# Performance work log

Hardware: AMD Instinct MI355X
Metric: run time of the kernel (lower is better)

The kernel has to match this reference:

```python
import jax, jax.numpy as jnp
import numpy as np

NEG_SLOPE = 0.2

def _gatv2_layer(x, src, tgt, Wl, Wr, att, bias, num_nodes, heads, ch):
    # x: [N, Fin]; src/tgt: [E] (self loops already included)
    xl = (x @ Wl).reshape(num_nodes, heads, ch)  # source transform [N,H,C]
    xr = (x @ Wr).reshape(num_nodes, heads, ch)  # target transform [N,H,C]
    m = xl[src] + xr[tgt]                        # [E,H,C]
    m = jnp.where(m > 0, m, NEG_SLOPE * m)       # LeakyReLU
    e = jnp.einsum('ehc,hc->eh', m, att)         # attention logits [E,H]
    # softmax over incoming edges of each target node (numerically stable)
    e_max = jax.ops.segment_max(e, tgt, num_segments=num_nodes)
    e_max = jnp.where(jnp.isfinite(e_max), e_max, 0.0)
    alpha = jnp.exp(e - e_max[tgt])              # [E,H]
    denom = jax.ops.segment_sum(alpha, tgt, num_segments=num_nodes)
    alpha = alpha / (denom[tgt] + 1e-16)
    out = jax.ops.segment_sum(alpha[:, :, None] * xl[src], tgt, num_segments=num_nodes)  # [N,H,C]
    return out.mean(axis=1) + bias               # concat=False -> mean over heads, then bias


def setup_inputs() -> dict:
    key = jax.random.key(0)
    ks = jax.random.split(key, 12)
    N, E = 50000, 800000
    IN, HID, H = 128, 64, 2
    features = jax.random.normal(ks[0], (N, IN), dtype=jnp.float32)
    edge_index = jax.random.randint(ks[1], (2, E), 0, N, dtype=jnp.int64)
    s = 0.1
    return {
        'features': features,
        'edge_index': edge_index,
        'Wl1': jax.random.normal(ks[2], (IN, H * HID), dtype=jnp.float32) * s,
        'Wr1': jax.random.normal(ks[3], (IN, H * HID), dtype=jnp.float32) * s,
        'att1': jax.random.normal(ks[4], (H, HID), dtype=jnp.float32) * s,
        'b1': jnp.zeros((HID,), dtype=jnp.float32),
        'Wl2': jax.random.normal(ks[5], (HID, H * HID), dtype=jnp.float32) * s,
        'Wr2': jax.random.normal(ks[6], (HID, H * HID), dtype=jnp.float32) * s,
        'att2': jax.random.normal(ks[7], (H, HID), dtype=jnp.float32) * s,
        'b2': jnp.zeros((HID,), dtype=jnp.float32),
    }


def reference(features, edge_index, Wl1, Wr1, att1, b1, Wl2, Wr2, att2, b2):
    N = features.shape[0]
    H, HID = att1.shape
    # PyG GATv2Conv default add_self_loops=True
    loop = jnp.arange(N, dtype=edge_index.dtype)
    src = jnp.concatenate([edge_index[0], loop])
    tgt = jnp.concatenate([edge_index[1], loop])
    h = _gatv2_layer(features, src, tgt, Wl1, Wr1, att1, b1, N, H, HID)
    h = jax.nn.relu(h)
    out = _gatv2_layer(h, src, tgt, Wl2, Wr2, att2, b2, N, H, HID)
    return out  # node_mask in original is None
```

## Files before the change

kernel.cpp:

```cpp
#include <hip/hip_runtime.h>
#include <hip/hip_bf16.h>
#include <math.h>


#define HEADS 2
#define CH 64
#define FDIM (HEADS * CH)
#define CAP 48
#define HBLK 3328

typedef _Float16 f16_t;
typedef _Float16 f16x4 __attribute__((ext_vector_type(4)));
typedef _Float16 f16x8 __attribute__((ext_vector_type(8)));
typedef float f32x4 __attribute__((ext_vector_type(4)));


__global__ __launch_bounds__(256)
void init_kernel(const float* __restrict__ Wl1, const float* __restrict__ Wr1,
                 const float* __restrict__ Wl2, const float* __restrict__ Wr2,
                 f16_t* __restrict__ fl1, f16_t* __restrict__ fr1,
                 f16_t* __restrict__ fl2, f16_t* __restrict__ fr2,
                 int* __restrict__ cnt, int N) {
    int bx = blockIdx.x;
    if (bx < 4) {
        const float* W; f16_t* F; int K;
        switch (bx) {
            case 0:  W = Wl1; F = fl1; K = 128; break;
            case 1:  W = Wr1; F = fr1; K = 128; break;
            case 2:  W = Wl2; F = fl2; K = 64;  break;
            default: W = Wr2; F = fr2; K = 64;  break;
        }
        int S = K >> 5;
        int total = 8 * S * 64;
        for (int idx = threadIdx.x; idx < total; idx += blockDim.x) {
            int l  = idx & 63;
            int ts = idx >> 6;
            int s  = ts % S;
            int t  = ts / S;
            int n  = t * 16 + (l & 15);
            int k0 = s * 32 + (l >> 4) * 8;
            f16x8 v;
            #pragma unroll
            for (int j = 0; j < 8; ++j) v[j] = (f16_t)W[(size_t)(k0 + j) * 128 + n];
            *(f16x8*)(F + (size_t)idx * 8) = v;
        }
    } else {
        int n4 = (N + 3) >> 2;
        int stride = (gridDim.x - 4) * blockDim.x;
        for (int i = (bx - 4) * blockDim.x + threadIdx.x; i < n4; i += stride) {
            int i0 = i * 4;
            if (i0 + 3 < N) *(int4*)(cnt + i0) = make_int4(0, 0, 0, 0);
            else for (int k = 0; k < 4 && i0 + k < N; ++k) cnt[i0 + k] = 0;
        }
    }
}


__device__ __forceinline__ unsigned int pack_bf16x2(float x, float y) {
    __hip_bfloat16 lo = __float2bfloat16(x);
    __hip_bfloat16 hi = __float2bfloat16(y);
    unsigned short ulo = *reinterpret_cast<unsigned short*>(&lo);
    unsigned short uhi = *reinterpret_cast<unsigned short*>(&hi);
    return ((unsigned int)uhi << 16) | ulo;
}

__device__ __forceinline__
void gemm_body(const float* __restrict__ X,
               const f16_t* __restrict__ FL, const f16_t* __restrict__ FR,
               unsigned int* __restrict__ Y0b, float* __restrict__ Y1,
               int N, int K, int gblk, float* lds_f) {
    f16_t* Af = (f16_t*)lds_f;
    int tid  = threadIdx.x;
    int lane = tid & 63;
    int wave = tid >> 6;
    int row0 = gblk * 32;
    int S = K >> 5;

    {
        int r  = tid >> 3;
        int m  = r & 15;
        int g  = r >> 4;
        int gr = row0 + r;
        int kc = (tid & 7) * (K >> 3);
        const float* xp = X + (size_t)gr * K + kc;
        f16_t* areg = Af + g * (16 * K);
        for (int c = 0; c < (K >> 3); c += 4) {
            float4 xv = make_float4(0.f, 0.f, 0.f, 0.f);
            if (gr < N) xv = *(const float4*)(xp + c);
            int k = kc + c;
            int s = k >> 5;
            int lanei = ((k >> 3) & 3) * 16 + m;
            int j = k & 7;
            f16x4 h;
            h[0] = (f16_t)xv.x; h[1] = (f16_t)xv.y;
            h[2] = (f16_t)xv.z; h[3] = (f16_t)xv.w;
            *(f16x4*)(areg + ((s * 64 + lanei) * 8 + j)) = h;
        }
    }
    __syncthreads();

    int rg  = wave >> 1;
    int mat = wave & 1;
    const f16_t* F = mat ? FR : FL;

    f32x4 acc[8];
    #pragma unroll
    for (int t = 0; t < 8; ++t) acc[t] = (f32x4){0.f, 0.f, 0.f, 0.f};

    const f16_t* aw = Af + rg * (16 * K);
    for (int s = 0; s < S; ++s) {
        f16x8 a = *(const f16x8*)(aw + (s * 64 + lane) * 8);
        #pragma unroll
        for (int t = 0; t < 8; ++t) {
            f16x8 b = *(const f16x8*)(F + ((size_t)(t * S + s) * 64 + lane) * 8);
            acc[t] = __builtin_amdgcn_mfma_f32_16x16x32_f16(a, b, acc[t], 0, 0, 0);
        }
    }
    __syncthreads();

    float* ew = lds_f + wave * (16 * 68);
    int mrow = (lane >> 4) * 4;
    int ccol = lane & 15;
    int rr = lane & 15;
    int ch = lane >> 4;
    int gr2 = row0 + rg * 16 + rr;

    #pragma unroll
    for (int h = 0; h < 2; ++h) {
        #pragma unroll
        for (int tt = 0; tt < 4; ++tt)
            #pragma unroll
            for (int r = 0; r < 4; ++r)
                ew[(mrow + r) * 68 + tt * 16 + ccol] = acc[h * 4 + tt][r];
        __syncthreads();
        if (gr2 < N) {
            const float* src = ew + rr * 68 + ch * 16;
            if (mat == 0) {
                uint4 o0, o1;
                o0.x = pack_bf16x2(src[0],  src[1]);
                o0.y = pack_bf16x2(src[2],  src[3]);
                o0.z = pack_bf16x2(src[4],  src[5]);
                o0.w = pack_bf16x2(src[6],  src[7]);
                o1.x = pack_bf16x2(src[8],  src[9]);
                o1.y = pack_bf16x2(src[10], src[11]);
                o1.z = pack_bf16x2(src[12], src[13]);
                o1.w = pack_bf16x2(src[14], src[15]);
                unsigned int* dst = Y0b + (size_t)gr2 * (FDIM / 2) + h * 32 + ch * 8;
                *(uint4*)dst       = o0;
                *(uint4*)(dst + 4) = o1;
            } else {
                float* dst = Y1 + (size_t)gr2 * FDIM + h * 64 + ch * 16;
                #pragma unroll
                for (int q = 0; q < 4; ++q)
                    *(float4*)(dst + q * 4) = *(const float4*)(src + q * 4);
            }
        }
        __syncthreads();
    }
}

__global__ __launch_bounds__(256)
void fused_scatter_gemm_kernel(const float* __restrict__ X,
                               const f16_t* __restrict__ FL,
                               const f16_t* __restrict__ FR,
                               unsigned int* __restrict__ Y0b,
                               float* __restrict__ Y1,
                               int N, int K,
                               const int* __restrict__ ei, int* __restrict__ cnt,
                               int* __restrict__ ssrc, int E) {
    __shared__ float lds_f[4352];

    if (blockIdx.x < HBLK) {
        int vb   = blockIdx.x;
        int part = vb & 7;
        int blk  = vb >> 3;
        int nblk = HBLK >> 3;
        int lo = (int)(((long long)N * part) >> 3);
        int hi = (int)(((long long)N * (part + 1)) >> 3);
        int stride = nblk * blockDim.x;
        int G = E >> 2;
        for (int g = blk * blockDim.x + threadIdx.x; g < G; g += stride) {
            int4 t4 = *(const int4*)(ei + E + g * 4);
            if (t4.x >= lo && t4.x < hi) {
                int k = atomicAdd(&cnt[t4.x], 1);
                if (k < CAP) ssrc[t4.x * CAP + k] = ei[g * 4 + 0];
            }
            if (t4.y >= lo && t4.y < hi) {
                int k = atomicAdd(&cnt[t4.y], 1);
                if (k < CAP) ssrc[t4.y * CAP + k] = ei[g * 4 + 1];
            }
            if (t4.z >= lo && t4.z < hi) {
                int k = atomicAdd(&cnt[t4.z], 1);
                if (k < CAP) ssrc[t4.z * CAP + k] = ei[g * 4 + 2];
            }
            if (t4.w >= lo && t4.w < hi) {
                int k = atomicAdd(&cnt[t4.w], 1);
                if (k < CAP) ssrc[t4.w * CAP + k] = ei[g * 4 + 3];
            }
        }
        for (int e = (G << 2) + blk * blockDim.x + threadIdx.x; e < E; e += stride) {
            int t = ei[E + e];
            if (t >= lo && t < hi) {
                int k = atomicAdd(&cnt[t], 1);
                if (k < CAP) ssrc[t * CAP + k] = ei[e];
            }
        }
        for (int n = lo + blk * blockDim.x + threadIdx.x; n < hi; n += stride) {
            int k = atomicAdd(&cnt[n], 1);
            if (k < CAP) ssrc[n * CAP + k] = n;
        }
        return;
    }

    gemm_body(X, FL, FR, Y0b, Y1, N, K, blockIdx.x - HBLK, lds_f);
}

__global__ __launch_bounds__(256)
void gemm_kernel(const float* __restrict__ X,
                 const f16_t* __restrict__ FL, const f16_t* __restrict__ FR,
                 unsigned int* __restrict__ Y0b, float* __restrict__ Y1,
                 int N, int K) {
    __shared__ float lds_f[4352];
    gemm_body(X, FL, FR, Y0b, Y1, N, K, blockIdx.x, lds_f);
}


__device__ __forceinline__ void unpack_bf16x2(unsigned int u, float& x, float& y) {
    x = __uint_as_float(u << 16);
    y = __uint_as_float(u & 0xFFFF0000u);
}

__device__ __forceinline__ float2 lrelu2(float2 t) {
    t.x = fmaxf(t.x, 0.2f * t.x);
    t.y = fmaxf(t.y, 0.2f * t.y);
    return t;
}

__device__ __forceinline__
float2 agg_node(const unsigned int* __restrict__ xlb, const float* __restrict__ xr,
                const int* __restrict__ cnt, const int* __restrict__ ssrc,
                float2 a2, int node, int lane) {
    float2 xr2 = *(const float2*)(xr + (size_t)node * FDIM + 2 * lane);

    int beg = node * CAP;
    int deg = cnt[node];
    deg = min(deg, CAP);
    int end = beg + deg;

    float l = 0.f;
    float2 acc = make_float2(0.f, 0.f);

    bool b0 = (lane & 1) != 0;
    bool b1 = (lane & 2) != 0;
    bool b2 = (lane & 4) != 0;
    int base = lane & 32;

    int i = beg;
    int n8 = beg + (deg & ~7);
    for (; i < n8; i += 8) {
        int s0 = ssrc[i + 0];
        int s1 = ssrc[i + 1];
        int s2 = ssrc[i + 2];
        int s3 = ssrc[i + 3];
        int s4 = ssrc[i + 4];
        int s5 = ssrc[i + 5];
        int s6 = ssrc[i + 6];
        int s7 = ssrc[i + 7];
        unsigned int u0 = xlb[(size_t)s0 * (FDIM / 2) + lane];
        unsigned int u1 = xlb[(size_t)s1 * (FDIM / 2) + lane];
        unsigned int u2 = xlb[(size_t)s2 * (FDIM / 2) + lane];
        unsigned int u3 = xlb[(size_t)s3 * (FDIM / 2) + lane];
        unsigned int u4 = xlb[(size_t)s4 * (FDIM / 2) + lane];
        unsigned int u5 = xlb[(size_t)s5 * (FDIM / 2) + lane];
        unsigned int u6 = xlb[(size_t)s6 * (FDIM / 2) + lane];
        unsigned int u7 = xlb[(size_t)s7 * (FDIM / 2) + lane];
        float2 v0, v1, v2, v3, v4, v5, v6, v7;
        unpack_bf16x2(u0, v0.x, v0.y);
        unpack_bf16x2(u1, v1.x, v1.y);
        unpack_bf16x2(u2, v2.x, v2.y);
        unpack_bf16x2(u3, v3.x, v3.y);
        unpack_bf16x2(u4, v4.x, v4.y);
        unpack_bf16x2(u5, v5.x, v5.y);
        unpack_bf16x2(u6, v6.x, v6.y);
        unpack_bf16x2(u7, v7.x, v7.y);

        float2 t0 = lrelu2(make_float2(v0.x + xr2.x, v0.y + xr2.y));
        float2 t1 = lrelu2(make_float2(v1.x + xr2.x, v1.y + xr2.y));
        float2 t2 = lrelu2(make_float2(v2.x + xr2.x, v2.y + xr2.y));
        float2 t3 = lrelu2(make_float2(v3.x + xr2.x, v3.y + xr2.y));
        float2 t4 = lrelu2(make_float2(v4.x + xr2.x, v4.y + xr2.y));
        float2 t5 = lrelu2(make_float2(v5.x + xr2.x, v5.y + xr2.y));
        float2 t6 = lrelu2(make_float2(v6.x + xr2.x, v6.y + xr2.y));
        float2 t7 = lrelu2(make_float2(v7.x + xr2.x, v7.y + xr2.y));
        float p0 = fmaf(t0.x, a2.x, t0.y * a2.y);
        float p1 = fmaf(t1.x, a2.x, t1.y * a2.y);
        float p2 = fmaf(t2.x, a2.x, t2.y * a2.y);
        float p3 = fmaf(t3.x, a2.x, t3.y * a2.y);
        float p4 = fmaf(t4.x, a2.x, t4.y * a2.y);
        float p5 = fmaf(t5.x, a2.x, t5.y * a2.y);
        float p6 = fmaf(t6.x, a2.x, t6.y * a2.y);
        float p7 = fmaf(t7.x, a2.x, t7.y * a2.y);

        float s01 = (b0 ? p1 : p0) + __shfl_xor(b0 ? p0 : p1, 1, 64);
        float s23 = (b0 ? p3 : p2) + __shfl_xor(b0 ? p2 : p3, 1, 64);
        float s45 = (b0 ? p5 : p4) + __shfl_xor(b0 ? p4 : p5, 1, 64);
        float s67 = (b0 ? p7 : p6) + __shfl_xor(b0 ? p6 : p7, 1, 64);
        float q03 = (b1 ? s23 : s01) + __shfl_xor(b1 ? s01 : s23, 2, 64);
        float q47 = (b1 ? s67 : s45) + __shfl_xor(b1 ? s45 : s67, 2, 64);
        float r = (b2 ? q47 : q03) + __shfl_xor(b2 ? q03 : q47, 4, 64);
        r += __shfl_xor(r, 8, 64);
        r += __shfl_xor(r, 16, 64);

        float a = __expf(r);
        float al0 = __shfl(a, base | 0, 64);
        float al1 = __shfl(a, base | 1, 64);
        float al2 = __shfl(a, base | 2, 64);
        float al3 = __shfl(a, base | 3, 64);
        float al4 = __shfl(a, base | 4, 64);
        float al5 = __shfl(a, base | 5, 64);
        float al6 = __shfl(a, base | 6, 64);
        float al7 = __shfl(a, base | 7, 64);

        acc.x = fmaf(al0, v0.x, acc.x); acc.y = fmaf(al0, v0.y, acc.y);
        acc.x = fmaf(al1, v1.x, acc.x); acc.y = fmaf(al1, v1.y, acc.y);
        acc.x = fmaf(al2, v2.x, acc.x); acc.y = fmaf(al2, v2.y, acc.y);
        acc.x = fmaf(al3, v3.x, acc.x); acc.y = fmaf(al3, v3.y, acc.y);
        acc.x = fmaf(al4, v4.x, acc.x); acc.y = fmaf(al4, v4.y, acc.y);
        acc.x = fmaf(al5, v5.x, acc.x); acc.y = fmaf(al5, v5.y, acc.y);
        acc.x = fmaf(al6, v6.x, acc.x); acc.y = fmaf(al6, v6.y, acc.y);
        acc.x = fmaf(al7, v7.x, acc.x); acc.y = fmaf(al7, v7.y, acc.y);
        l += ((al0 + al1) + (al2 + al3)) + ((al4 + al5) + (al6 + al7));
    }
    int n4 = i + ((end - i) & ~3);
    for (; i < n4; i += 4) {
        int s0 = ssrc[i + 0];
        int s1 = ssrc[i + 1];
        int s2 = ssrc[i + 2];
        int s3 = ssrc[i + 3];
        unsigned int u0 = xlb[(size_t)s0 * (FDIM / 2) + lane];
        unsigned int u1 = xlb[(size_t)s1 * (FDIM / 2) + lane];
        unsigned int u2 = xlb[(size_t)s2 * (FDIM / 2) + lane];
        unsigned int u3 = xlb[(size_t)s3 * (FDIM / 2) + lane];
        float2 v0, v1, v2, v3;
        unpack_bf16x2(u0, v0.x, v0.y);
        unpack_bf16x2(u1, v1.x, v1.y);
        unpack_bf16x2(u2, v2.x, v2.y);
        unpack_bf16x2(u3, v3.x, v3.y);

        float2 t0 = lrelu2(make_float2(v0.x + xr2.x, v0.y + xr2.y));
        float2 t1 = lrelu2(make_float2(v1.x + xr2.x, v1.y + xr2.y));
        float2 t2 = lrelu2(make_float2(v2.x + xr2.x, v2.y + xr2.y));
        float2 t3 = lrelu2(make_float2(v3.x + xr2.x, v3.y + xr2.y));
        float p0 = fmaf(t0.x, a2.x, t0.y * a2.y);
        float p1 = fmaf(t1.x, a2.x, t1.y * a2.y);
        float p2 = fmaf(t2.x, a2.x, t2.y * a2.y);
        float p3 = fmaf(t3.x, a2.x, t3.y * a2.y);

        float s01 = (b0 ? p1 : p0) + __shfl_xor(b0 ? p0 : p1, 1, 64);
        float s23 = (b0 ? p3 : p2) + __shfl_xor(b0 ? p2 : p3, 1, 64);
        float q = (b1 ? s23 : s01) + __shfl_xor(b1 ? s01 : s23, 2, 64);
        q += __shfl_xor(q, 4, 64);
        q += __shfl_xor(q, 8, 64);
        q += __shfl_xor(q, 16, 64);
        float a = __expf(q);
        float al0 = __shfl(a, base | 0, 64);
        float al1 = __shfl(a, base | 1, 64);
        float al2 = __shfl(a, base | 2, 64);
        float al3 = __shfl(a, base | 3, 64);

        acc.x = fmaf(al0, v0.x, acc.x); acc.y = fmaf(al0, v0.y, acc.y);
        acc.x = fmaf(al1, v1.x, acc.x); acc.y = fmaf(al1, v1.y, acc.y);
        acc.x = fmaf(al2, v2.x, acc.x); acc.y = fmaf(al2, v2.y, acc.y);
        acc.x = fmaf(al3, v3.x, acc.x); acc.y = fmaf(al3, v3.y, acc.y);
        l += (al0 + al1) + (al2 + al3);
    }
    for (; i < end; ++i) {
        int s = ssrc[i];
        unsigned int u = xlb[(size_t)s * (FDIM / 2) + lane];
        float2 v;
        unpack_bf16x2(u, v.x, v.y);
        float2 t = lrelu2(make_float2(v.x + xr2.x, v.y + xr2.y));
        float p = fmaf(t.x, a2.x, t.y * a2.y);
        #pragma unroll
        for (int d = 1; d < 32; d <<= 1) p += __shfl_xor(p, d, 64);
        float al = __expf(p);
        acc.x = fmaf(al, v.x, acc.x);
        acc.y = fmaf(al, v.y, acc.y);
        l += al;
    }

    float inv = 1.0f / (l + 1e-16f);
    return make_float2(acc.x * inv, acc.y * inv);
}

__global__ __launch_bounds__(256)
void agg_kernel(const unsigned int* __restrict__ xlb, const float* __restrict__ xr,
                const int* __restrict__ cnt, const int* __restrict__ ssrc,
                const float* __restrict__ att, const float* __restrict__ bias,
                float* __restrict__ out, int N, int do_relu) {
    int node = blockIdx.x * 4 + (threadIdx.x >> 6);
    int lane = threadIdx.x & 63;
    if (node >= N) return;

    float2 a2 = *(const float2*)(att + 2 * lane);
    float2 r = agg_node(xlb, xr, cnt, ssrc, a2, node, lane);
    float ox = 0.5f * (r.x + __shfl_xor(r.x, 32, 64));
    float oy = 0.5f * (r.y + __shfl_xor(r.y, 32, 64));
    if (lane < 32) {
        float2 b = *(const float2*)(bias + 2 * lane);
        ox += b.x; oy += b.y;
        if (do_relu) { ox = fmaxf(ox, 0.f); oy = fmaxf(oy, 0.f); }
        *(float2*)(out + (size_t)node * CH + 2 * lane) = make_float2(ox, oy);
    }
}


__global__ __launch_bounds__(256)
void agg_gemm_kernel(const unsigned int* __restrict__ xlb, const float* __restrict__ xr,
                     const int* __restrict__ cnt, const int* __restrict__ ssrc,
                     const float* __restrict__ att, const float* __restrict__ bias,
                     const f16_t* __restrict__ FL, const f16_t* __restrict__ FR,
                     unsigned int* __restrict__ Y0b, float* __restrict__ Y1, int N) {
    __shared__ float lds_f[4352];
    __shared__ float hrows[32 * 68];
    const int K = 64;
    const int S = 2;

    int tid  = threadIdx.x;
    int lane = tid & 63;
    int wave = tid >> 6;
    int row0 = blockIdx.x * 32;

    float2 a2 = *(const float2*)(att + 2 * lane);
    float2 bv = make_float2(0.f, 0.f);
    if (lane < 32) bv = *(const float2*)(bias + 2 * lane);

    for (int q = 0; q < 8; ++q) {
        int ln   = wave * 8 + q;
        int node = row0 + ln;
        float ox = 0.f, oy = 0.f;
        if (node < N) {
            float2 r = agg_node(xlb, xr, cnt, ssrc, a2, node, lane);
            ox = 0.5f * (r.x + __shfl_xor(r.x, 32, 64));
            oy = 0.5f * (r.y + __shfl_xor(r.y, 32, 64));
            ox = fmaxf(ox + bv.x, 0.f);
            oy = fmaxf(oy + bv.y, 0.f);
        }
        if (lane < 32)
            *(float2*)(hrows + ln * 68 + 2 * lane) = make_float2(ox, oy);
    }
    __syncthreads();

    f16_t* Af = (f16_t*)lds_f;
    {
        int r  = tid >> 3;
        int m  = r & 15;
        int g  = r >> 4;
        int kc = (tid & 7) * 8;
        const float* xp = hrows + r * 68 + kc;
        f16_t* areg = Af + g * (16 * K);
        #pragma unroll
        for (int c = 0; c < 8; c += 4) {
            float4 xv = *(const float4*)(xp + c);
            int k = kc + c;
            int s = k >> 5;
            int lanei = ((k >> 3) & 3) * 16 + m;
            int j = k & 7;
            f16x4 h;
            h[0] = (f16_t)xv.x; h[1] = (f16_t)xv.y;
            h[2] = (f16_t)xv.z; h[3] = (f16_t)xv.w;
            *(f16x4*)(areg + ((s * 64 + lanei) * 8 + j)) = h;
        }
    }
    __syncthreads();

    int rg  = wave >> 1;
    int mat = wave & 1;
    const f16_t* F = mat ? FR : FL;

    f32x4 acc[8];
    #pragma unroll
    for (int t = 0; t < 8; ++t) acc[t] = (f32x4){0.f, 0.f, 0.f, 0.f};

    const f16_t* aw = Af + rg * (16 * K);
    #pragma unroll
    for (int s = 0; s < S; ++s) {
        f16x8 a = *(const f16x8*)(aw + (s * 64 + lane) * 8);
        #pragma unroll
        for (int t = 0; t < 8; ++t) {
            f16x8 b = *(const f16x8*)(F + ((size_t)(t * S + s) * 64 + lane) * 8);
            acc[t] = __builtin_amdgcn_mfma_f32_16x16x32_f16(a, b, acc[t], 0, 0, 0);
        }
    }
    __syncthreads();

    float* ew = lds_f + wave * (16 * 68);
    int mrow = (lane >> 4) * 4;
    int ccol = lane & 15;
    int rr = lane & 15;
    int ch = lane >> 4;
    int gr2 = row0 + rg * 16 + rr;

    #pragma unroll
    for (int h = 0; h < 2; ++h) {
        #pragma unroll
        for (int tt = 0; tt < 4; ++tt)
            #pragma unroll
            for (int r = 0; r < 4; ++r)
                ew[(mrow + r) * 68 + tt * 16 + ccol] = acc[h * 4 + tt][r];
        __syncthreads();
        if (gr2 < N) {
            const float* src = ew + rr * 68 + ch * 16;
            if (mat == 0) {
                uint4 o0, o1;
                o0.x = pack_bf16x2(src[0],  src[1]);
                o0.y = pack_bf16x2(src[2],  src[3]);
                o0.z = pack_bf16x2(src[4],  src[5]);
                o0.w = pack_bf16x2(src[6],  src[7]);
                o1.x = pack_bf16x2(src[8],  src[9]);
                o1.y = pack_bf16x2(src[10], src[11]);
                o1.z = pack_bf16x2(src[12], src[13]);
                o1.w = pack_bf16x2(src[14], src[15]);
                unsigned int* dst = Y0b + (size_t)gr2 * (FDIM / 2) + h * 32 + ch * 8;
                *(uint4*)dst       = o0;
                *(uint4*)(dst + 4) = o1;
            } else {
                float* dst = Y1 + (size_t)gr2 * FDIM + h * 64 + ch * 16;
                #pragma unroll
                for (int q = 0; q < 4; ++q)
                    *(float4*)(dst + q * 4) = *(const float4*)(src + q * 4);
            }
        }
        __syncthreads();
    }
}


static inline size_t align_up(size_t x, size_t a) { return (x + a - 1) & ~(a - 1); }

extern "C" void kernel_launch(void* const* d_in, const int* in_sizes, int n_in,
                              void* d_out, int out_size, void* d_ws, size_t ws_size,
                              hipStream_t stream) {
    const float* features = (const float*)d_in[0];
    const int*   ei       = (const int*)d_in[1];
    const float* Wl1      = (const float*)d_in[2];
    const float* Wr1      = (const float*)d_in[3];
    const float* att1     = (const float*)d_in[4];
    const float* b1       = (const float*)d_in[5];
    const float* Wl2      = (const float*)d_in[6];
    const float* Wr2      = (const float*)d_in[7];
    const float* att2     = (const float*)d_in[8];
    const float* b2       = (const float*)d_in[9];

    int N = in_sizes[0] / FDIM;
    int E = in_sizes[1] / 2;

    size_t sz_cnt  = align_up((size_t)N * 4, 256);
    size_t sz_ssrc = align_up((size_t)N * CAP * 4, 256);
    size_t sz_xlb  = align_up((size_t)N * (FDIM / 2) * 4, 256);
    size_t sz_xr   = align_up((size_t)N * FDIM * 4, 256);
    size_t sz_h    = align_up((size_t)N * CH * 4, 256);
    size_t sz_f128 = align_up((size_t)8 * 4 * 64 * 8 * 2, 256);
    size_t sz_f64  = align_up((size_t)8 * 2 * 64 * 8 * 2, 256);

    char* w = (char*)d_ws;
    int* cnt          = (int*)w;          w += sz_cnt;
    int* ssrc         = (int*)w;          w += sz_ssrc;
    unsigned int* xlb = (unsigned int*)w; w += sz_xlb;
    float* xr         = (float*)w;        w += sz_xr;

    size_t need_fused = sz_cnt + sz_ssrc + 2 * sz_xlb + 2 * sz_xr
                      + 2 * sz_f128 + 2 * sz_f64;

    int gblocks = (N + 31) / 32;
    dim3 agrid((N + 3) / 4);

    if (ws_size >= need_fused) {
        unsigned int* xlb2 = (unsigned int*)w; w += sz_xlb;
        float* xr2         = (float*)w;        w += sz_xr;
        f16_t* fl1 = (f16_t*)w; w += sz_f128;
        f16_t* fr1 = (f16_t*)w; w += sz_f128;
        f16_t* fl2 = (f16_t*)w; w += sz_f64;
        f16_t* fr2 = (f16_t*)w; w += sz_f64;

        init_kernel<<<56, 256, 0, stream>>>(Wl1, Wr1, Wl2, Wr2,
                                            fl1, fr1, fl2, fr2, cnt, N);
        fused_scatter_gemm_kernel<<<HBLK + gblocks, 256, 0, stream>>>(
            features, fl1, fr1, xlb, xr, N, 128, ei, cnt, ssrc, E);
        agg_gemm_kernel<<<gblocks, 256, 0, stream>>>(
            xlb, xr, cnt, ssrc, att1, b1, fl2, fr2, xlb2, xr2, N);
        agg_kernel<<<agrid, 256, 0, stream>>>(
            xlb2, xr2, cnt, ssrc, att2, b2, (float*)d_out, N, 0);
    } else {
        float* hbuf = (float*)w; w += sz_h;
        f16_t* fl1 = (f16_t*)w; w += sz_f128;
        f16_t* fr1 = (f16_t*)w; w += sz_f128;
        f16_t* fl2 = (f16_t*)w; w += sz_f64;
        f16_t* fr2 = (f16_t*)w; w += sz_f64;

        init_kernel<<<56, 256, 0, stream>>>(Wl1, Wr1, Wl2, Wr2,
                                            fl1, fr1, fl2, fr2, cnt, N);
        fused_scatter_gemm_kernel<<<HBLK + gblocks, 256, 0, stream>>>(
            features, fl1, fr1, xlb, xr, N, 128, ei, cnt, ssrc, E);
        agg_kernel<<<agrid, 256, 0, stream>>>(xlb, xr, cnt, ssrc, att1, b1, hbuf, N, 1);
        gemm_kernel<<<gblocks, 256, 0, stream>>>(hbuf, fl2, fr2, xlb, xr, N, 64);
        agg_kernel<<<agrid, 256, 0, stream>>>(xlb, xr, cnt, ssrc, att2, b2, (float*)d_out, N, 0);
    }
}
```

Measured before the change: 275.4 us.

## Restructure fused aggregate+GEMM to 16-row tiles with 8 waves, direct MFMA stores

The layer-1 aggregate-plus-layer-2-GEMM kernel now handles 16 nodes per block with 512 threads, so each wave aggregates 2 nodes instead of 8 and there are twice as many blocks. Each wave computes two 16x16 output tiles and writes them straight from MFMA registers to global memory, which removes the LDS staging buffer and the extra barriers. The edge-index loads in the aggregation loops are also vectorized to int4. The cost is narrower, scattered global stores and less reuse of weight fragments per block.

```diff
diff --git a/kernel.cpp b/kernel.cpp
--- a/kernel.cpp
+++ b/kernel.cpp
@@ -258,14 +258,10 @@
     int i = beg;
     int n8 = beg + (deg & ~7);
     for (; i < n8; i += 8) {
-        int s0 = ssrc[i + 0];
-        int s1 = ssrc[i + 1];
-        int s2 = ssrc[i + 2];
-        int s3 = ssrc[i + 3];
-        int s4 = ssrc[i + 4];
-        int s5 = ssrc[i + 5];
-        int s6 = ssrc[i + 6];
-        int s7 = ssrc[i + 7];
+        int4 sA = *(const int4*)(ssrc + i);
+        int4 sB = *(const int4*)(ssrc + i + 4);
+        int s0 = sA.x, s1 = sA.y, s2 = sA.z, s3 = sA.w;
+        int s4 = sB.x, s5 = sB.y, s6 = sB.z, s7 = sB.w;
         unsigned int u0 = xlb[(size_t)s0 * (FDIM / 2) + lane];
         unsigned int u1 = xlb[(size_t)s1 * (FDIM / 2) + lane];
         unsigned int u2 = xlb[(size_t)s2 * (FDIM / 2) + lane];
@@ -333,10 +329,8 @@
     }
     int n4 = i + ((end - i) & ~3);
     for (; i < n4; i += 4) {
-        int s0 = ssrc[i + 0];
-        int s1 = ssrc[i + 1];
-        int s2 = ssrc[i + 2];
-        int s3 = ssrc[i + 3];
+        int4 sA = *(const int4*)(ssrc + i);
+        int s0 = sA.x, s1 = sA.y, s2 = sA.z, s3 = sA.w;
         unsigned int u0 = xlb[(size_t)s0 * (FDIM / 2) + lane];
         unsigned int u1 = xlb[(size_t)s1 * (FDIM / 2) + lane];
         unsigned int u2 = xlb[(size_t)s2 * (FDIM / 2) + lane];
@@ -415,28 +409,27 @@
 }
 
 
-__global__ __launch_bounds__(256)
-void agg_gemm_kernel(const unsigned int* __restrict__ xlb, const float* __restrict__ xr,
-                     const int* __restrict__ cnt, const int* __restrict__ ssrc,
-                     const float* __restrict__ att, const float* __restrict__ bias,
-                     const f16_t* __restrict__ FL, const f16_t* __restrict__ FR,
-                     unsigned int* __restrict__ Y0b, float* __restrict__ Y1, int N) {
-    __shared__ float lds_f[4352];
-    __shared__ float hrows[32 * 68];
-    const int K = 64;
-    const int S = 2;
+__global__ __launch_bounds__(512)
+void agg_gemm16_kernel(const unsigned int* __restrict__ xlb, const float* __restrict__ xr,
+                       const int* __restrict__ cnt, const int* __restrict__ ssrc,
+                       const float* __restrict__ att, const float* __restrict__ bias,
+                       const f16_t* __restrict__ FL, const f16_t* __restrict__ FR,
+                       unsigned int* __restrict__ Y0b, float* __restrict__ Y1, int N) {
+    __shared__ float hrows[16 * 68];
+    __shared__ f16_t Af[16 * 64];
 
     int tid  = threadIdx.x;
     int lane = tid & 63;
     int wave = tid >> 6;
-    int row0 = blockIdx.x * 32;
+    int row0 = blockIdx.x * 16;
 
     float2 a2 = *(const float2*)(att + 2 * lane);
     float2 bv = make_float2(0.f, 0.f);
     if (lane < 32) bv = *(const float2*)(bias + 2 * lane);
 
-    for (int q = 0; q < 8; ++q) {
-        int ln   = wave * 8 + q;
+    #pragma unroll 1
+    for (int q = 0; q < 2; ++q) {
+        int ln   = wave * 2 + q;
         int node = row0 + ln;
         float ox = 0.f, oy = 0.f;
         if (node < N) {
@@ -451,87 +444,63 @@
     }
     __syncthreads();
 
-    f16_t* Af = (f16_t*)lds_f;
-    {
+    if (tid < 128) {
         int r  = tid >> 3;
-        int m  = r & 15;
-        int g  = r >> 4;
         int kc = (tid & 7) * 8;
         const float* xp = hrows + r * 68 + kc;
-        f16_t* areg = Af + g * (16 * K);
         #pragma unroll
         for (int c = 0; c < 8; c += 4) {
             float4 xv = *(const float4*)(xp + c);
             int k = kc + c;
             int s = k >> 5;
-            int lanei = ((k >> 3) & 3) * 16 + m;
+            int lanei = ((k >> 3) & 3) * 16 + r;
             int j = k & 7;
             f16x4 h;
             h[0] = (f16_t)xv.x; h[1] = (f16_t)xv.y;
             h[2] = (f16_t)xv.z; h[3] = (f16_t)xv.w;
-            *(f16x4*)(areg + ((s * 64 + lanei) * 8 + j)) = h;
+            *(f16x4*)(Af + ((s * 64 + lanei) * 8 + j)) = h;
         }
     }
     __syncthreads();
 
-    int rg  = wave >> 1;
     int mat = wave & 1;
+    int pp  = wave >> 1;
     const f16_t* F = mat ? FR : FL;
-
-    f32x4 acc[8];
-    #pragma unroll
-    for (int t = 0; t < 8; ++t) acc[t] = (f32x4){0.f, 0.f, 0.f, 0.f};
-
-    const f16_t* aw = Af + rg * (16 * K);
+    const int S = 2;
+
+    f32x4 acc0 = (f32x4){0.f, 0.f, 0.f, 0.f};
+    f32x4 acc1 = (f32x4){0.f, 0.f, 0.f, 0.f};
     #pragma unroll
     for (int s = 0; s < S; ++s) {
-        f16x8 a = *(const f16x8*)(aw + (s * 64 + lane) * 8);
-        #pragma unroll
-        for (int t = 0; t < 8; ++t) {
-            f16x8 b = *(const f16x8*)(F + ((size_t)(t * S + s) * 64 + lane) * 8);
-            acc[t] = __builtin_amdgcn_mfma_f32_16x16x32_f16(a, b, acc[t], 0, 0, 0);
-        }
-    }
-    __syncthreads();
-
-    float* ew = lds_f + wave * (16 * 68);
+        f16x8 a  = *(const f16x8*)(Af + (s * 64 + lane) * 8);
+        f16x8 b0 = *(const f16x8*)(F + ((size_t)((pp * 2 + 0) * S + s) * 64 + lane) * 8);
+        f16x8 b1 = *(const f16x8*)(F + ((size_t)((pp * 2 + 1) * S + s) * 64 + lane) * 8);
+        acc0 = __builtin_amdgcn_mfma_f32_16x16x32_f16(a, b0, acc0, 0, 0, 0);
+        acc1 = __builtin_amdgcn_mfma_f32_16x16x32_f16(a, b1, acc1, 0, 0, 0);
+    }
+
     int mrow = (lane >> 4) * 4;
     int ccol = lane & 15;
-    int rr = lane & 15;
-    int ch = lane >> 4;
-    int gr2 = row0 + rg * 16 + rr;
-
     #pragma unroll
-    for (int h = 0; h < 2; ++h) {
+    for (int u = 0; u < 2; ++u) {
+        int t = pp * 2 + u;
+        f32x4 av = u ? acc1 : acc0;
         #pragma unroll
-        for (int tt = 0; tt < 4; ++tt)
-            #pragma unroll
-            for (int r = 0; r < 4; ++r)
-                ew[(mrow + r) * 68 + tt * 16 + ccol] = acc[h * 4 + tt][r];
-        __syncthreads();
-        if (gr2 < N) {
-            const float* src = ew + rr * 68 + ch * 16;
-            if (mat == 0) {
-                uint4 o0, o1;
-                o0.x = pack_bf16x2(src[0],  src[1]);
-                o0.y = pack_bf16x2(src[2],  src[3]);
-                o0.z = pack_bf16x2(src[4],  src[5]);
-                o0.w = pack_bf16x2(src[6],  src[7]);
-                o1.x = pack_bf16x2(src[8],  src[9]);
-                o1.y = pack_bf16x2(src[10], src[11]);
-                o1.z = pack_bf16x2(src[12], src[13]);
-                o1.w = pack_bf16x2(src[14], src[15]);
-                unsigned int* dst = Y0b + (size_t)gr2 * (FDIM / 2) + h * 32 + ch * 8;
-                *(uint4*)dst       = o0;
-                *(uint4*)(dst + 4) = o1;
-            } else {
-                float* dst = Y1 + (size_t)gr2 * FDIM + h * 64 + ch * 16;
-                #pragma unroll
-                for (int q = 0; q < 4; ++q)
-                    *(float4*)(dst + q * 4) = *(const float4*)(src + q * 4);
-            }
-        }
-        __syncthreads();
+        for (int r = 0; r < 4; ++r) {
+            float v = av[r];
+            float w = __shfl_xor(v, 1, 64);
+            int grow = row0 + mrow + r;
+            if (grow < N) {
+                if (mat == 0) {
+                    if (!(lane & 1)) {
+                        unsigned int uu = pack_bf16x2(v, w);
+                        Y0b[(size_t)grow * (FDIM / 2) + t * 8 + (ccol >> 1)] = uu;
+                    }
+                } else {
+                    Y1[(size_t)grow * FDIM + t * 16 + ccol] = v;
+                }
+            }
+        }
     }
 }
 
@@ -583,11 +552,13 @@
         f16_t* fl2 = (f16_t*)w; w += sz_f64;
         f16_t* fr2 = (f16_t*)w; w += sz_f64;
 
+        int g16 = (N + 15) / 16;
+
         init_kernel<<<56, 256, 0, stream>>>(Wl1, Wr1, Wl2, Wr2,
                                             fl1, fr1, fl2, fr2, cnt, N);
         fused_scatter_gemm_kernel<<<HBLK + gblocks, 256, 0, stream>>>(
             features, fl1, fr1, xlb, xr, N, 128, ei, cnt, ssrc, E);
-        agg_gemm_kernel<<<gblocks, 256, 0, stream>>>(
+        agg_gemm16_kernel<<<g16, 512, 0, stream>>>(
             xlb, xr, cnt, ssrc, att1, b1, fl2, fr2, xlb2, xr2, N);
         agg_kernel<<<agrid, 256, 0, stream>>>(
             xlb2, xr2, cnt, ssrc, att2, b2, (float*)d_out, N, 0);
```

Result: no change. 271.1 us (-1.6%).
